# Optimization experiments

Hardware: AMD Instinct MI355X
Metric: run time of the kernel (lower is better)

The kernel has to match this reference:

```python
import jax, jax.numpy as jnp
import numpy as np

B, S, H, NH = 2, 384, 768, 12
DPH = H // NH
SCALE = 1.0 / np.sqrt(DPH)


def _layer_norm(x, g, b, eps=1e-6):
    m = jnp.mean(x, axis=-1, keepdims=True)
    v = jnp.mean(jnp.square(x - m), axis=-1, keepdims=True)
    return (x - m) * jax.lax.rsqrt(v + eps) * g + b


def setup_inputs() -> dict:
    key = jax.random.key(0)
    ks = jax.random.split(key, 12)
    std = 0.02
    return {
        "hidden_states": jax.random.normal(ks[0], (B, S, H), jnp.float32),
        "attention_mask": jnp.ones((B, S), jnp.int32),
        "rel_pos_embedding": jax.random.normal(ks[1], (B, S, S, H), jnp.float32),
        "Wq": jax.random.normal(ks[2], (H, H), jnp.float32) * std,
        "bq": jnp.zeros((H,), jnp.float32),
        "Wk": jax.random.normal(ks[3], (H, H), jnp.float32) * std,
        "bk": jnp.zeros((H,), jnp.float32),
        "Wv": jax.random.normal(ks[4], (H, H), jnp.float32) * std,
        "bv": jnp.zeros((H,), jnp.float32),
        "Wr": jax.random.normal(ks[5], (H, H), jnp.float32) * std,
        "br": jnp.zeros((H,), jnp.float32),
        "u": jax.random.normal(ks[6], (NH, DPH), jnp.float32) * std,
        "v": jax.random.normal(ks[7], (NH, DPH), jnp.float32) * std,
        "Wf": jax.random.normal(ks[8], (H, H), jnp.float32) * std,
        "bf": jnp.zeros((H,), jnp.float32),
        "ln_g": jnp.ones((H,), jnp.float32),
        "ln_b": jnp.zeros((H,), jnp.float32),
    }


def reference(hidden_states, attention_mask, rel_pos_embedding,
              Wq, bq, Wk, bk, Wv, bv, Wr, br, u, v, Wf, bf, ln_g, ln_b):
    # projections (torch Linear: x @ W.T + b)
    def heads(x):  # [B,S,H] -> [B,NH,S,DPH]
        return x.reshape(B, S, NH, DPH).transpose(0, 2, 1, 3)
    q = heads(hidden_states @ Wq.T + bq)
    k = heads(hidden_states @ Wk.T + bk)
    val = heads(hidden_states @ Wv.T + bv)
    # relative embedding projection: [B,S,S,H] -> [B,S,S,NH,DPH]
    rel = (rel_pos_embedding @ Wr.T + br).reshape(B, S, S, NH, DPH)

    # Transformer-XL style decomposition
    AC = jnp.einsum('bhid,bhjd->bhij', q + u[None, :, None, :], k)
    Bp = jnp.einsum('bhid,bijhd->bhij', q, rel)
    Dp = jnp.einsum('hd,bijhd->bhij', v, rel)
    scores = (AC + Bp + Dp) * SCALE

    # 2-D mask -> [B,1,1,S]
    ext = (1.0 - attention_mask[:, None, None, :].astype(scores.dtype)) * (-1e18)
    probs = jax.nn.softmax(scores + ext, axis=-1)  # dropout is identity at eval

    ctx = jnp.einsum('bhij,bhjd->bhid', probs, val)
    ctx = ctx.transpose(0, 2, 1, 3).reshape(B, S, H)
    out = ctx @ Wf.T + bf
    return _layer_norm(out + hidden_states, ln_g, ln_b)
```

## Files before the change

### kernel.cpp

```cpp
#include <hip/hip_runtime.h>
#include <cstddef>
#include <cstdint>

static constexpr int BB   = 2;
static constexpr int SS   = 384;
static constexpr int HH   = 768;
static constexpr int NHD  = 12;
static constexpr int ROWS = BB * SS;
#define SCALE_F 0.125f

typedef __attribute__((ext_vector_type(8))) short short8;
typedef __attribute__((ext_vector_type(4))) float f32x4;

static __device__ __forceinline__ unsigned short f2bf(float x) {
    unsigned int b = __float_as_uint(x);
    b = (b + 0x7fffu + ((b >> 16) & 1u)) >> 16;
    return (unsigned short)b;
}

__global__ __launch_bounds__(256) void k_tobf(const float* __restrict__ s0,
                                              const float* __restrict__ s1,
                                              const float* __restrict__ s2,
                                              const float* __restrict__ s3,
                                              const float* __restrict__ s4,
                                              unsigned short* __restrict__ d0,
                                              unsigned short* __restrict__ d1,
                                              unsigned short* __restrict__ d2,
                                              unsigned short* __restrict__ d3,
                                              unsigned short* __restrict__ d4) {
    const int z = blockIdx.y;
    const float* s = (z == 0) ? s0 : (z == 1) ? s1 : (z == 2) ? s2 : (z == 3) ? s3 : s4;
    unsigned short* d = (z == 0) ? d0 : (z == 1) ? d1 : (z == 2) ? d2 : (z == 3) ? d3 : d4;
    const int t = blockIdx.x * 256 + threadIdx.x;
    const float4 v = *(const float4*)&s[(size_t)t * 4];
    ushort4 o;
    o.x = f2bf(v.x); o.y = f2bf(v.y); o.z = f2bf(v.z); o.w = f2bf(v.w);
    *(ushort4*)&d[(size_t)t * 4] = o;
}

template<bool ADD>
__device__ __forceinline__ void mfma_gemm_body(const unsigned short* __restrict__ A,
                                               const unsigned short* __restrict__ W,
                                               const float* __restrict__ bias,
                                               const float* __restrict__ addsrc,
                                               float* __restrict__ C) {
    const int tid = threadIdx.x;
    const int wid = tid >> 6, lane = tid & 63;
    const int i0 = blockIdx.y * 64, o0 = blockIdx.x * 64;
    const int wr = (wid >> 1) * 32, wc = (wid & 1) * 32;
    const int lrow = lane & 15;
    const int kgrp = (lane >> 4) * 8;

    const unsigned short* Ar0 = A + (size_t)(i0 + wr + lrow) * HH + kgrp;
    const unsigned short* Ar1 = Ar0 + 16 * HH;
    const unsigned short* Wr0 = W + (size_t)(o0 + wc + lrow) * HH + kgrp;
    const unsigned short* Wr1 = Wr0 + 16 * HH;

    f32x4 acc00 = {0.f, 0.f, 0.f, 0.f}, acc01 = {0.f, 0.f, 0.f, 0.f};
    f32x4 acc10 = {0.f, 0.f, 0.f, 0.f}, acc11 = {0.f, 0.f, 0.f, 0.f};
#pragma unroll 4
    for (int k0 = 0; k0 < HH; k0 += 32) {
        const short8 a0 = *(const short8*)(Ar0 + k0);
        const short8 a1 = *(const short8*)(Ar1 + k0);
        const short8 b0 = *(const short8*)(Wr0 + k0);
        const short8 b1 = *(const short8*)(Wr1 + k0);
        acc00 = __builtin_amdgcn_mfma_f32_16x16x32_bf16(a0, b0, acc00, 0, 0, 0);
        acc01 = __builtin_amdgcn_mfma_f32_16x16x32_bf16(a0, b1, acc01, 0, 0, 0);
        acc10 = __builtin_amdgcn_mfma_f32_16x16x32_bf16(a1, b0, acc10, 0, 0, 0);
        acc11 = __builtin_amdgcn_mfma_f32_16x16x32_bf16(a1, b1, acc11, 0, 0, 0);
    }

    const int rbase = (lane >> 4) * 4;
#pragma unroll
    for (int tr = 0; tr < 2; tr++) {
#pragma unroll
        for (int tc = 0; tc < 2; tc++) {
            const f32x4 a = (tr == 0) ? ((tc == 0) ? acc00 : acc01)
                                      : ((tc == 0) ? acc10 : acc11);
            const int col = o0 + wc + tc * 16 + lrow;
            const float bv = bias[col];
#pragma unroll
            for (int r = 0; r < 4; r++) {
                const int row = i0 + wr + tr * 16 + rbase + r;
                float v = a[r] + bv;
                if (ADD) v += addsrc[(size_t)row * HH + col];
                C[(size_t)row * HH + col] = v;
            }
        }
    }
}

__global__ __launch_bounds__(256) void k_gemm_qkv(const unsigned short* __restrict__ A,
                                                  const unsigned short* __restrict__ Wq, const float* __restrict__ bq,
                                                  const unsigned short* __restrict__ Wk, const float* __restrict__ bk,
                                                  const unsigned short* __restrict__ Wv, const float* __restrict__ bv,
                                                  float* __restrict__ qo, float* __restrict__ ko,
                                                  float* __restrict__ vo) {
    const int z = blockIdx.z;
    const unsigned short* W = (z == 0) ? Wq : (z == 1) ? Wk : Wv;
    const float* bias = (z == 0) ? bq : (z == 1) ? bk : bv;
    float* C = (z == 0) ? qo : (z == 1) ? ko : vo;
    mfma_gemm_body<false>(A, W, bias, nullptr, C);
}

__global__ __launch_bounds__(256) void k_gemm_out(const unsigned short* __restrict__ A,
                                                  const unsigned short* __restrict__ W,
                                                  const float* __restrict__ bias,
                                                  const float* __restrict__ addsrc,
                                                  float* __restrict__ C) {
    mfma_gemm_body<true>(A, W, bias, addsrc, C);
}

__global__ __launch_bounds__(256) void k_uproj(const float* __restrict__ q,
                                               const float* __restrict__ Wr,
                                               const float* __restrict__ vhead,
                                               const float* __restrict__ br,
                                               unsigned short* __restrict__ U,
                                               float* __restrict__ cb) {
    const int h = blockIdx.z;
    const int e0 = blockIdx.x * 64, r0 = blockIdx.y * 64;
    __shared__ float qT[64][68];
    __shared__ float wE[64][68];
    const int tid = threadIdx.x;
    const int lr = tid >> 2;
    const int bc = (tid & 3) * 16;
#pragma unroll
    for (int m = 0; m < 4; m++) {
        const int col = bc + m * 4;
        const float4 qv = *(const float4*)&q[(size_t)(r0 + lr) * HH + h * 64 + col];
        const float4 vv = *(const float4*)&vhead[h * 64 + col];
        qT[col + 0][lr] = qv.x + vv.x;
        qT[col + 1][lr] = qv.y + vv.y;
        qT[col + 2][lr] = qv.z + vv.z;
        qT[col + 3][lr] = qv.w + vv.w;
        const float4 wv = *(const float4*)&Wr[(size_t)(h * 64 + lr) * HH + e0 + col];
        *(float4*)&wE[lr][col] = wv;
    }
    __syncthreads();
    const int tr = (tid >> 4) << 2;
    const int tc = (tid & 15) << 2;
    float acc[4][4] = {};
#pragma unroll 8
    for (int d = 0; d < 64; d++) {
        const float4 a4 = *(const float4*)&qT[d][tr];
        const float4 b4 = *(const float4*)&wE[d][tc];
        const float ab[4] = {a4.x, a4.y, a4.z, a4.w};
        const float bb[4] = {b4.x, b4.y, b4.z, b4.w};
#pragma unroll
        for (int r = 0; r < 4; r++)
#pragma unroll
            for (int c = 0; c < 4; c++)
                acc[r][c] = fmaf(ab[r], bb[c], acc[r][c]);
    }
#pragma unroll
    for (int r = 0; r < 4; r++) {
        ushort4 o;
        o.x = f2bf(acc[r][0]); o.y = f2bf(acc[r][1]);
        o.z = f2bf(acc[r][2]); o.w = f2bf(acc[r][3]);
        *(ushort4*)&U[(size_t)(r0 + tr + r) * (NHD * HH) + (size_t)h * HH + e0 + tc] = o;
    }
    if (e0 == 0 && tid < 64) {
        float s = 0.f;
        for (int d = 0; d < 64; d++)
            s = fmaf(qT[d][tid], br[h * 64 + d], s);
        cb[(r0 + tid) * NHD + h] = s;
    }
}

__global__ __launch_bounds__(256) void k_ac(const float* __restrict__ q,
                                            const float* __restrict__ kk,
                                            const float* __restrict__ uvec,
                                            const float* __restrict__ cb,
                                            float* __restrict__ sc) {
    const int bh = blockIdx.z;
    const int b = bh / NHD, h = bh - b * NHD;
    const int i0 = blockIdx.y * 64, j0 = blockIdx.x * 64;
    __shared__ float qT[64][68];
    __shared__ float kT[64][68];
    const int tid = threadIdx.x;
    const int lr = tid >> 2;
    const int bc = (tid & 3) * 16;
#pragma unroll
    for (int m = 0; m < 4; m++) {
        const int col = bc + m * 4;
        const float4 qv = *(const float4*)&q[(size_t)(b * SS + i0 + lr) * HH + h * 64 + col];
        const float4 uv = *(const float4*)&uvec[h * 64 + col];
        qT[col + 0][lr] = qv.x + uv.x;
        qT[col + 1][lr] = qv.y + uv.y;
        qT[col + 2][lr] = qv.z + uv.z;
        qT[col + 3][lr] = qv.w + uv.w;
        const float4 kv = *(const float4*)&kk[(size_t)(b * SS + j0 + lr) * HH + h * 64 + col];
        kT[col + 0][lr] = kv.x;
        kT[col + 1][lr] = kv.y;
        kT[col + 2][lr] = kv.z;
        kT[col + 3][lr] = kv.w;
    }
    __syncthreads();
    const int tr = (tid >> 4) << 2;
    const int tc = (tid & 15) << 2;
    float acc[4][4] = {};
#pragma unroll 8
    for (int d = 0; d < 64; d++) {
        const float4 a4 = *(const float4*)&qT[d][tr];
        const float4 b4 = *(const float4*)&kT[d][tc];
        const float ab[4] = {a4.x, a4.y, a4.z, a4.w};
        const float bb[4] = {b4.x, b4.y, b4.z, b4.w};
#pragma unroll
        for (int r = 0; r < 4; r++)
#pragma unroll
            for (int c = 0; c < 4; c++)
                acc[r][c] = fmaf(ab[r], bb[c], acc[r][c]);
    }
#pragma unroll
    for (int r = 0; r < 4; r++) {
        const int i = i0 + tr + r;
        const float cbr = cb[(b * SS + i) * NHD + h];
        float4 o;
        o.x = acc[r][0] + cbr; o.y = acc[r][1] + cbr;
        o.z = acc[r][2] + cbr; o.w = acc[r][3] + cbr;
        *(float4*)&sc[((size_t)(b * SS + i) * NHD + h) * SS + j0 + tc] = o;
    }
}

__global__ __launch_bounds__(256) void k_bd(const float* __restrict__ rpe,
                                            const unsigned short* __restrict__ U,
                                            const int* __restrict__ mask,
                                            float* __restrict__ scP) {
    const int i = blockIdx.x;
    const int b = blockIdx.y;
    const int row = b * SS + i;
    const int tid = threadIdx.x;

    __shared__ unsigned short Ul[NHD * HH];
    __shared__ float sc[NHD][392];
    __shared__ float extl[SS];

    float* plane = scP + (size_t)row * NHD * SS;

    {
        const uint4* Ur = (const uint4*)(U + (size_t)row * NHD * HH);
        uint4* Uld = (uint4*)Ul;
        for (int t = tid; t < NHD * HH / 8; t += 256) Uld[t] = Ur[t];
        for (int t = tid; t < NHD * 96; t += 256) {
            const int h = t / 96, c4 = (t - h * 96) << 2;
            *(float4*)&sc[h][c4] = *(const float4*)&plane[h * SS + c4];
        }
        for (int t = tid; t < SS; t += 256)
            extl[t] = (1.0f - (float)mask[b * SS + t]) * (-1e18f);
    }
    __syncthreads();

    const int wave = tid >> 6;
    const int lane = tid & 63;

    {
        const int jsub = lane >> 3;
        const int elane = lane & 7;
        const float* rrow = rpe + (size_t)row * SS * HH;

        for (int g = wave; g < 12; g += 4) {
            const int jbase = g * 32 + jsub;
            const float* rp0 = rrow + (size_t)jbase * HH + (elane << 2);
            float acc[4][NHD] = {};
#pragma unroll 2
            for (int ec = 0; ec < 24; ec++) {
                const int eo = ec << 5;
                const float4 t0 = *(const float4*)(rp0 + eo);
                const float4 t1 = *(const float4*)(rp0 + eo + 8 * HH);
                const float4 t2 = *(const float4*)(rp0 + eo + 16 * HH);
                const float4 t3 = *(const float4*)(rp0 + eo + 24 * HH);
                const float rb[4][4] = {{t0.x, t0.y, t0.z, t0.w},
                                        {t1.x, t1.y, t1.z, t1.w},
                                        {t2.x, t2.y, t2.z, t2.w},
                                        {t3.x, t3.y, t3.z, t3.w}};
                const int uo = eo + (elane << 2);
#pragma unroll
                for (int h = 0; h < NHD; h++) {
                    const uint2 w2 = *(const uint2*)&Ul[h * HH + uo];
                    float ub[4];
                    ub[0] = __uint_as_float(w2.x << 16);
                    ub[1] = __uint_as_float(w2.x & 0xffff0000u);
                    ub[2] = __uint_as_float(w2.y << 16);
                    ub[3] = __uint_as_float(w2.y & 0xffff0000u);
#pragma unroll
                    for (int rr = 0; rr < 4; rr++)
#pragma unroll
                        for (int c = 0; c < 4; c++)
                            acc[rr][h] = fmaf(rb[rr][c], ub[c], acc[rr][h]);
                }
            }
#pragma unroll
            for (int rr = 0; rr < 4; rr++)
#pragma unroll
                for (int h = 0; h < NHD; h++) {
                    float a = acc[rr][h];
                    a += __shfl_xor(a, 1);
                    a += __shfl_xor(a, 2);
                    a += __shfl_xor(a, 4);
                    acc[rr][h] = a;
                }
            if (elane == 0) {
#pragma unroll
                for (int rr = 0; rr < 4; rr++) {
                    const int j = jbase + (rr << 3);
#pragma unroll
                    for (int h = 0; h < NHD; h++)
                        sc[h][j] += acc[rr][h];
                }
            }
        }
    }
    __syncthreads();

    {
        for (int h = wave; h < NHD; h += 4) {
            float vbuf[6];
            float m = -1e30f;
#pragma unroll
            for (int t2 = 0; t2 < 6; t2++) {
                vbuf[t2] = sc[h][lane + t2 * 64] * SCALE_F + extl[lane + t2 * 64];
                m = fmaxf(m, vbuf[t2]);
            }
#pragma unroll
            for (int off = 1; off < 64; off <<= 1) m = fmaxf(m, __shfl_xor(m, off));
            float ssum = 0.f;
#pragma unroll
            for (int t2 = 0; t2 < 6; t2++) {
                const float e = __expf(vbuf[t2] - m);
                vbuf[t2] = e;
                ssum += e;
            }
#pragma unroll
            for (int off = 1; off < 64; off <<= 1) ssum += __shfl_xor(ssum, off);
            const float inv = 1.0f / ssum;
#pragma unroll
            for (int t2 = 0; t2 < 6; t2++)
                plane[h * SS + lane + t2 * 64] = vbuf[t2] * inv;
        }
    }
}

__global__ __launch_bounds__(256) void k_pv(const float* __restrict__ P,
                                            const float* __restrict__ val,
                                            unsigned short* __restrict__ ctxb) {
    const int bh = blockIdx.y;
    const int b = bh / NHD, h = bh - b * NHD;
    const int i0 = blockIdx.x * 64;
    __shared__ float pT[64][68];
    __shared__ float vB[64][68];
    const int tid = threadIdx.x;
    const int lr = tid >> 2;
    const int bc = (tid & 3) * 16;
    const int tr = (tid >> 4) << 2;
    const int tc = (tid & 15) << 2;

    float4 pv[4], vv[4];
#pragma unroll
    for (int m = 0; m < 4; m++) {
        const int col = bc + m * 4;
        pv[m] = *(const float4*)&P[((size_t)(b * SS + i0 + lr) * NHD + h) * SS + col];
        vv[m] = *(const float4*)&val[(size_t)(b * SS + lr) * HH + h * 64 + col];
    }
    float acc[4][4] = {};
    for (int jt = 0; jt < SS; jt += 64) {
        __syncthreads();
#pragma unroll
        for (int m = 0; m < 4; m++) {
            const int col = bc + m * 4;
            pT[col + 0][lr] = pv[m].x; pT[col + 1][lr] = pv[m].y;
            pT[col + 2][lr] = pv[m].z; pT[col + 3][lr] = pv[m].w;
            *(float4*)&vB[lr][col] = vv[m];
        }
        __syncthreads();
        if (jt + 64 < SS) {
#pragma unroll
            for (int m = 0; m < 4; m++) {
                const int col = bc + m * 4;
                pv[m] = *(const float4*)&P[((size_t)(b * SS + i0 + lr) * NHD + h) * SS + jt + 64 + col];
                vv[m] = *(const float4*)&val[(size_t)(b * SS + jt + 64 + lr) * HH + h * 64 + col];
            }
        }
#pragma unroll 8
        for (int jj = 0; jj < 64; jj++) {
            const float4 a4 = *(const float4*)&pT[jj][tr];
            const float4 b4 = *(const float4*)&vB[jj][tc];
            const float ab[4] = {a4.x, a4.y, a4.z, a4.w};
            const float bb[4] = {b4.x, b4.y, b4.z, b4.w};
#pragma unroll
            for (int r = 0; r < 4; r++)
#pragma unroll
                for (int c = 0; c < 4; c++)
                    acc[r][c] = fmaf(ab[r], bb[c], acc[r][c]);
        }
    }
#pragma unroll
    for (int r = 0; r < 4; r++) {
        ushort4 o;
        o.x = f2bf(acc[r][0]); o.y = f2bf(acc[r][1]);
        o.z = f2bf(acc[r][2]); o.w = f2bf(acc[r][3]);
        *(ushort4*)&ctxb[(size_t)(b * SS + i0 + tr + r) * HH + h * 64 + tc] = o;
    }
}

__global__ __launch_bounds__(256) void k_ln(const float* __restrict__ x,
                                            const float* __restrict__ g,
                                            const float* __restrict__ bta,
                                            float* __restrict__ o) {
    const int row = blockIdx.x;
    const int tid = threadIdx.x;
    const float* xr = x + (size_t)row * HH;
    __shared__ float red[4];
    const float v0 = xr[tid], v1 = xr[tid + 256], v2 = xr[tid + 512];
    float s = v0 + v1 + v2;
#pragma unroll
    for (int off = 1; off < 64; off <<= 1) s += __shfl_xor(s, off);
    if ((tid & 63) == 0) red[tid >> 6] = s;
    __syncthreads();
    const float mean = (red[0] + red[1] + red[2] + red[3]) * (1.0f / 768.0f);
    const float d0 = v0 - mean, d1 = v1 - mean, d2 = v2 - mean;
    float sq = d0 * d0 + d1 * d1 + d2 * d2;
#pragma unroll
    for (int off = 1; off < 64; off <<= 1) sq += __shfl_xor(sq, off);
    __syncthreads();
    if ((tid & 63) == 0) red[tid >> 6] = sq;
    __syncthreads();
    const float var = (red[0] + red[1] + red[2] + red[3]) * (1.0f / 768.0f);
    const float inv = rsqrtf(var + 1e-6f);
    o[(size_t)row * HH + tid]       = d0 * inv * g[tid]       + bta[tid];
    o[(size_t)row * HH + tid + 256] = d1 * inv * g[tid + 256] + bta[tid + 256];
    o[(size_t)row * HH + tid + 512] = d2 * inv * g[tid + 512] + bta[tid + 512];
}

extern "C" void kernel_launch(void* const* d_in, const int* in_sizes, int n_in,
                              void* d_out, int out_size, void* d_ws, size_t ws_size,
                              hipStream_t stream) {
    (void)in_sizes; (void)n_in; (void)out_size; (void)ws_size;
    const float* hs   = (const float*)d_in[0];
    const int*   mask = (const int*)d_in[1];
    const float* rpe  = (const float*)d_in[2];
    const float* Wq = (const float*)d_in[3];  const float* bq = (const float*)d_in[4];
    const float* Wk = (const float*)d_in[5];  const float* bk = (const float*)d_in[6];
    const float* Wv = (const float*)d_in[7];  const float* bv = (const float*)d_in[8];
    const float* Wr = (const float*)d_in[9];  const float* br = (const float*)d_in[10];
    const float* u  = (const float*)d_in[11]; const float* v  = (const float*)d_in[12];
    const float* Wf = (const float*)d_in[13]; const float* bf = (const float*)d_in[14];
    const float* lng = (const float*)d_in[15]; const float* lnb = (const float*)d_in[16];
    float* out = (float*)d_out;

    const size_t MAT = (size_t)ROWS * HH;
    float* wsf     = (float*)d_ws;
    float* q_ws    = wsf;
    float* k_ws    = q_ws   + MAT;
    float* v_ws    = k_ws   + MAT;
    float* lnin_ws = v_ws   + MAT;
    float* cb_ws   = lnin_ws + MAT;
    float* sc_ws   = cb_ws  + (size_t)ROWS * NHD;
    unsigned short* U_ws   = (unsigned short*)(sc_ws + (size_t)ROWS * NHD * SS);
    unsigned short* hs_b   = U_ws + (size_t)ROWS * NHD * HH;
    unsigned short* Wq_b   = hs_b + MAT;
    unsigned short* Wk_b   = Wq_b + MAT;
    unsigned short* Wv_b   = Wk_b + MAT;
    unsigned short* Wf_b   = Wv_b + MAT;
    unsigned short* ctx_b  = Wf_b + MAT;

    k_tobf<<<dim3(576, 5), 256, 0, stream>>>(hs, Wq, Wk, Wv, Wf,
                                             hs_b, Wq_b, Wk_b, Wv_b, Wf_b);
    k_gemm_qkv<<<dim3(12, 12, 3), 256, 0, stream>>>(hs_b, Wq_b, bq, Wk_b, bk, Wv_b, bv,
                                                    q_ws, k_ws, v_ws);
    k_uproj<<<dim3(12, 12, 12), 256, 0, stream>>>(q_ws, Wr, v, br, U_ws, cb_ws);
    k_ac<<<dim3(6, 6, 24), 256, 0, stream>>>(q_ws, k_ws, u, cb_ws, sc_ws);
    k_bd<<<dim3(SS, BB), 256, 0, stream>>>(rpe, U_ws, mask, sc_ws);
    k_pv<<<dim3(6, 24), 256, 0, stream>>>(sc_ws, v_ws, ctx_b);
    k_gemm_out<<<dim3(12, 12), 256, 0, stream>>>(ctx_b, Wf_b, bf, hs, lnin_ws);
    k_ln<<<dim3(768), 256, 0, stream>>>(lnin_ws, lng, lnb, out);
}
```

Baseline: 283.5 us.

## Port uproj, AC and PV stages to bf16 MFMA with bf16 intermediates

Replaces the fp32 FMA shared-memory tiles in the U-projection, AC score and P·V kernels with bf16 MFMA 16x16x32 tiles. The QKV GEMM now emits bf16 q+u, q+v, k and a transposed V directly, and Wr is transposed to bf16 in the conversion kernel. The cb bias term moves to a small separate kernel, and probabilities are written as bf16 for the PV stage. This cuts fp32 ALU work and intermediate memory traffic, at the cost of more bf16 rounding in the attention path.

```diff
diff --git a/kernel.cpp b/kernel.cpp
--- a/kernel.cpp
+++ b/kernel.cpp
@@ -17,33 +17,60 @@
     b = (b + 0x7fffu + ((b >> 16) & 1u)) >> 16;
     return (unsigned short)b;
 }
+static __device__ __forceinline__ float bf2f(unsigned short u) {
+    return __uint_as_float((unsigned int)u << 16);
+}
 
 __global__ __launch_bounds__(256) void k_tobf(const float* __restrict__ s0,
                                               const float* __restrict__ s1,
                                               const float* __restrict__ s2,
                                               const float* __restrict__ s3,
                                               const float* __restrict__ s4,
+                                              const float* __restrict__ Wr,
                                               unsigned short* __restrict__ d0,
                                               unsigned short* __restrict__ d1,
                                               unsigned short* __restrict__ d2,
                                               unsigned short* __restrict__ d3,
-                                              unsigned short* __restrict__ d4) {
+                                              unsigned short* __restrict__ d4,
+                                              unsigned short* __restrict__ WrT) {
+    __shared__ float t[32][33];
     const int z = blockIdx.y;
-    const float* s = (z == 0) ? s0 : (z == 1) ? s1 : (z == 2) ? s2 : (z == 3) ? s3 : s4;
-    unsigned short* d = (z == 0) ? d0 : (z == 1) ? d1 : (z == 2) ? d2 : (z == 3) ? d3 : d4;
-    const int t = blockIdx.x * 256 + threadIdx.x;
-    const float4 v = *(const float4*)&s[(size_t)t * 4];
-    ushort4 o;
-    o.x = f2bf(v.x); o.y = f2bf(v.y); o.z = f2bf(v.z); o.w = f2bf(v.w);
-    *(ushort4*)&d[(size_t)t * 4] = o;
-}
-
-template<bool ADD>
-__device__ __forceinline__ void mfma_gemm_body(const unsigned short* __restrict__ A,
-                                               const unsigned short* __restrict__ W,
-                                               const float* __restrict__ bias,
-                                               const float* __restrict__ addsrc,
-                                               float* __restrict__ C) {
+    if (z < 5) {
+        const float* s = (z == 0) ? s0 : (z == 1) ? s1 : (z == 2) ? s2 : (z == 3) ? s3 : s4;
+        unsigned short* d = (z == 0) ? d0 : (z == 1) ? d1 : (z == 2) ? d2 : (z == 3) ? d3 : d4;
+        const int tt = blockIdx.x * 256 + threadIdx.x;
+        const float4 v = *(const float4*)&s[(size_t)tt * 4];
+        ushort4 o;
+        o.x = f2bf(v.x); o.y = f2bf(v.y); o.z = f2bf(v.z); o.w = f2bf(v.w);
+        *(ushort4*)&d[(size_t)tt * 4] = o;
+    } else {
+        const int tile = blockIdx.x;
+        const int tr_ = tile / 24, tc_ = tile % 24;
+        const int r = threadIdx.x >> 3, c4 = (threadIdx.x & 7) * 4;
+        const float4 v = *(const float4*)&Wr[(size_t)(tr_ * 32 + r) * HH + tc_ * 32 + c4];
+        t[r][c4 + 0] = v.x; t[r][c4 + 1] = v.y; t[r][c4 + 2] = v.z; t[r][c4 + 3] = v.w;
+        __syncthreads();
+        ushort4 o;
+        o.x = f2bf(t[c4 + 0][r]); o.y = f2bf(t[c4 + 1][r]);
+        o.z = f2bf(t[c4 + 2][r]); o.w = f2bf(t[c4 + 3][r]);
+        *(ushort4*)&WrT[(size_t)(tc_ * 32 + r) * HH + tr_ * 32 + c4] = o;
+    }
+}
+
+__global__ __launch_bounds__(256) void k_gemm_qkv(const unsigned short* __restrict__ A,
+                                                  const unsigned short* __restrict__ Wqb, const float* __restrict__ bq,
+                                                  const unsigned short* __restrict__ Wkb, const float* __restrict__ bk,
+                                                  const unsigned short* __restrict__ Wvb, const float* __restrict__ bv,
+                                                  const float* __restrict__ uvec,
+                                                  const float* __restrict__ vvec,
+                                                  unsigned short* __restrict__ qu_b,
+                                                  unsigned short* __restrict__ qv_b,
+                                                  unsigned short* __restrict__ k_b,
+                                                  unsigned short* __restrict__ vT_b) {
+    const int z = blockIdx.z;
+    const unsigned short* W = (z == 0) ? Wqb : (z == 1) ? Wkb : Wvb;
+    const float* bias = (z == 0) ? bq : (z == 1) ? bk : bv;
+
     const int tid = threadIdx.x;
     const int wid = tid >> 6, lane = tid & 63;
     const int i0 = blockIdx.y * 64, o0 = blockIdx.x * 64;
@@ -56,8 +83,8 @@
     const unsigned short* Wr0 = W + (size_t)(o0 + wc + lrow) * HH + kgrp;
     const unsigned short* Wr1 = Wr0 + 16 * HH;
 
-    f32x4 acc00 = {0.f, 0.f, 0.f, 0.f}, acc01 = {0.f, 0.f, 0.f, 0.f};
-    f32x4 acc10 = {0.f, 0.f, 0.f, 0.f}, acc11 = {0.f, 0.f, 0.f, 0.f};
+    f32x4 acc00 = {0.f,0.f,0.f,0.f}, acc01 = {0.f,0.f,0.f,0.f};
+    f32x4 acc10 = {0.f,0.f,0.f,0.f}, acc11 = {0.f,0.f,0.f,0.f};
 #pragma unroll 4
     for (int k0 = 0; k0 < HH; k0 += 32) {
         const short8 a0 = *(const short8*)(Ar0 + k0);
@@ -78,154 +105,149 @@
             const f32x4 a = (tr == 0) ? ((tc == 0) ? acc00 : acc01)
                                       : ((tc == 0) ? acc10 : acc11);
             const int col = o0 + wc + tc * 16 + lrow;
-            const float bv = bias[col];
-#pragma unroll
-            for (int r = 0; r < 4; r++) {
-                const int row = i0 + wr + tr * 16 + rbase + r;
-                float v = a[r] + bv;
-                if (ADD) v += addsrc[(size_t)row * HH + col];
-                C[(size_t)row * HH + col] = v;
-            }
-        }
-    }
-}
-
-__global__ __launch_bounds__(256) void k_gemm_qkv(const unsigned short* __restrict__ A,
-                                                  const unsigned short* __restrict__ Wq, const float* __restrict__ bq,
-                                                  const unsigned short* __restrict__ Wk, const float* __restrict__ bk,
-                                                  const unsigned short* __restrict__ Wv, const float* __restrict__ bv,
-                                                  float* __restrict__ qo, float* __restrict__ ko,
-                                                  float* __restrict__ vo) {
-    const int z = blockIdx.z;
-    const unsigned short* W = (z == 0) ? Wq : (z == 1) ? Wk : Wv;
-    const float* bias = (z == 0) ? bq : (z == 1) ? bk : bv;
-    float* C = (z == 0) ? qo : (z == 1) ? ko : vo;
-    mfma_gemm_body<false>(A, W, bias, nullptr, C);
-}
-
-__global__ __launch_bounds__(256) void k_gemm_out(const unsigned short* __restrict__ A,
-                                                  const unsigned short* __restrict__ W,
-                                                  const float* __restrict__ bias,
-                                                  const float* __restrict__ addsrc,
-                                                  float* __restrict__ C) {
-    mfma_gemm_body<true>(A, W, bias, addsrc, C);
-}
-
-__global__ __launch_bounds__(256) void k_uproj(const float* __restrict__ q,
-                                               const float* __restrict__ Wr,
-                                               const float* __restrict__ vhead,
-                                               const float* __restrict__ br,
-                                               unsigned short* __restrict__ U,
-                                               float* __restrict__ cb) {
+            const float bvv = bias[col];
+            if (z == 0) {
+                const float uu = uvec[col], vv = vvec[col];
+#pragma unroll
+                for (int r = 0; r < 4; r++) {
+                    const int row = i0 + wr + tr * 16 + rbase + r;
+                    const float val = a[r] + bvv;
+                    qu_b[(size_t)row * HH + col] = f2bf(val + uu);
+                    qv_b[(size_t)row * HH + col] = f2bf(val + vv);
+                }
+            } else if (z == 1) {
+#pragma unroll
+                for (int r = 0; r < 4; r++) {
+                    const int row = i0 + wr + tr * 16 + rbase + r;
+                    k_b[(size_t)row * HH + col] = f2bf(a[r] + bvv);
+                }
+            } else {
+                const int row0 = i0 + wr + tr * 16 + rbase;
+                const int bb2 = row0 / SS;
+                const int jj0 = row0 - bb2 * SS;
+                const int h2 = col >> 6, d2 = col & 63;
+                ushort4 o;
+                o.x = f2bf(a[0] + bvv); o.y = f2bf(a[1] + bvv);
+                o.z = f2bf(a[2] + bvv); o.w = f2bf(a[3] + bvv);
+                *(ushort4*)&vT_b[((size_t)(bb2 * NHD + h2) * 64 + d2) * SS + jj0] = o;
+            }
+        }
+    }
+}
+
+__global__ void k_cb(const unsigned short* __restrict__ qv,
+                     const float* __restrict__ br, float* __restrict__ cb) {
+    const int t = blockIdx.x * 256 + threadIdx.x;
+    if (t >= ROWS * NHD) return;
+    const int row = t / NHD, h = t - row * NHD;
+    float s = 0.f;
+    for (int d = 0; d < 64; d++)
+        s = fmaf(bf2f(qv[(size_t)row * HH + h * 64 + d]), br[h * 64 + d], s);
+    cb[t] = s;
+}
+
+__global__ __launch_bounds__(256) void k_uproj(const unsigned short* __restrict__ qv,
+                                               const unsigned short* __restrict__ WrT,
+                                               unsigned short* __restrict__ U) {
     const int h = blockIdx.z;
     const int e0 = blockIdx.x * 64, r0 = blockIdx.y * 64;
-    __shared__ float qT[64][68];
-    __shared__ float wE[64][68];
-    const int tid = threadIdx.x;
-    const int lr = tid >> 2;
-    const int bc = (tid & 3) * 16;
-#pragma unroll
-    for (int m = 0; m < 4; m++) {
-        const int col = bc + m * 4;
-        const float4 qv = *(const float4*)&q[(size_t)(r0 + lr) * HH + h * 64 + col];
-        const float4 vv = *(const float4*)&vhead[h * 64 + col];
-        qT[col + 0][lr] = qv.x + vv.x;
-        qT[col + 1][lr] = qv.y + vv.y;
-        qT[col + 2][lr] = qv.z + vv.z;
-        qT[col + 3][lr] = qv.w + vv.w;
-        const float4 wv = *(const float4*)&Wr[(size_t)(h * 64 + lr) * HH + e0 + col];
-        *(float4*)&wE[lr][col] = wv;
-    }
-    __syncthreads();
-    const int tr = (tid >> 4) << 2;
-    const int tc = (tid & 15) << 2;
-    float acc[4][4] = {};
-#pragma unroll 8
-    for (int d = 0; d < 64; d++) {
-        const float4 a4 = *(const float4*)&qT[d][tr];
-        const float4 b4 = *(const float4*)&wE[d][tc];
-        const float ab[4] = {a4.x, a4.y, a4.z, a4.w};
-        const float bb[4] = {b4.x, b4.y, b4.z, b4.w};
-#pragma unroll
-        for (int r = 0; r < 4; r++)
-#pragma unroll
-            for (int c = 0; c < 4; c++)
-                acc[r][c] = fmaf(ab[r], bb[c], acc[r][c]);
-    }
-#pragma unroll
-    for (int r = 0; r < 4; r++) {
-        ushort4 o;
-        o.x = f2bf(acc[r][0]); o.y = f2bf(acc[r][1]);
-        o.z = f2bf(acc[r][2]); o.w = f2bf(acc[r][3]);
-        *(ushort4*)&U[(size_t)(r0 + tr + r) * (NHD * HH) + (size_t)h * HH + e0 + tc] = o;
-    }
-    if (e0 == 0 && tid < 64) {
-        float s = 0.f;
-        for (int d = 0; d < 64; d++)
-            s = fmaf(qT[d][tid], br[h * 64 + d], s);
-        cb[(r0 + tid) * NHD + h] = s;
-    }
-}
-
-__global__ __launch_bounds__(256) void k_ac(const float* __restrict__ q,
-                                            const float* __restrict__ kk,
-                                            const float* __restrict__ uvec,
+    const int tid = threadIdx.x;
+    const int wid = tid >> 6, lane = tid & 63;
+    const int wr = (wid >> 1) * 32, wc = (wid & 1) * 32;
+    const int lrow = lane & 15;
+    const int kgrp = (lane >> 4) * 8;
+
+    const unsigned short* Ar0 = qv + (size_t)(r0 + wr + lrow) * HH + h * 64 + kgrp;
+    const unsigned short* Ar1 = Ar0 + 16 * HH;
+    const unsigned short* Br0 = WrT + (size_t)(e0 + wc + lrow) * HH + h * 64 + kgrp;
+    const unsigned short* Br1 = Br0 + 16 * HH;
+
+    f32x4 acc00 = {0.f,0.f,0.f,0.f}, acc01 = {0.f,0.f,0.f,0.f};
+    f32x4 acc10 = {0.f,0.f,0.f,0.f}, acc11 = {0.f,0.f,0.f,0.f};
+#pragma unroll
+    for (int k0 = 0; k0 < 64; k0 += 32) {
+        const short8 a0 = *(const short8*)(Ar0 + k0);
+        const short8 a1 = *(const short8*)(Ar1 + k0);
+        const short8 b0 = *(const short8*)(Br0 + k0);
+        const short8 b1 = *(const short8*)(Br1 + k0);
+        acc00 = __builtin_amdgcn_mfma_f32_16x16x32_bf16(a0, b0, acc00, 0, 0, 0);
+        acc01 = __builtin_amdgcn_mfma_f32_16x16x32_bf16(a0, b1, acc01, 0, 0, 0);
+        acc10 = __builtin_amdgcn_mfma_f32_16x16x32_bf16(a1, b0, acc10, 0, 0, 0);
+        acc11 = __builtin_amdgcn_mfma_f32_16x16x32_bf16(a1, b1, acc11, 0, 0, 0);
+    }
+
+    const int rbase = (lane >> 4) * 4;
+#pragma unroll
+    for (int tr = 0; tr < 2; tr++) {
+#pragma unroll
+        for (int tc = 0; tc < 2; tc++) {
+            const f32x4 a = (tr == 0) ? ((tc == 0) ? acc00 : acc01)
+                                      : ((tc == 0) ? acc10 : acc11);
+            const int e = e0 + wc + tc * 16 + lrow;
+#pragma unroll
+            for (int r = 0; r < 4; r++) {
+                const int row = r0 + wr + tr * 16 + rbase + r;
+                U[(size_t)row * (NHD * HH) + (size_t)h * HH + e] = f2bf(a[r]);
+            }
+        }
+    }
+}
+
+__global__ __launch_bounds__(256) void k_ac(const unsigned short* __restrict__ qu,
+                                            const unsigned short* __restrict__ kb,
                                             const float* __restrict__ cb,
                                             float* __restrict__ sc) {
     const int bh = blockIdx.z;
     const int b = bh / NHD, h = bh - b * NHD;
     const int i0 = blockIdx.y * 64, j0 = blockIdx.x * 64;
-    __shared__ float qT[64][68];
-    __shared__ float kT[64][68];
-    const int tid = threadIdx.x;
-    const int lr = tid >> 2;
-    const int bc = (tid & 3) * 16;
-#pragma unroll
-    for (int m = 0; m < 4; m++) {
-        const int col = bc + m * 4;
-        const float4 qv = *(const float4*)&q[(size_t)(b * SS + i0 + lr) * HH + h * 64 + col];
-        const float4 uv = *(const float4*)&uvec[h * 64 + col];
-        qT[col + 0][lr] = qv.x + uv.x;
-        qT[col + 1][lr] = qv.y + uv.y;
-        qT[col + 2][lr] = qv.z + uv.z;
-        qT[col + 3][lr] = qv.w + uv.w;
-        const float4 kv = *(const float4*)&kk[(size_t)(b * SS + j0 + lr) * HH + h * 64 + col];
-        kT[col + 0][lr] = kv.x;
-        kT[col + 1][lr] = kv.y;
-        kT[col + 2][lr] = kv.z;
-        kT[col + 3][lr] = kv.w;
-    }
-    __syncthreads();
-    const int tr = (tid >> 4) << 2;
-    const int tc = (tid & 15) << 2;
-    float acc[4][4] = {};
-#pragma unroll 8
-    for (int d = 0; d < 64; d++) {
-        const float4 a4 = *(const float4*)&qT[d][tr];
-        const float4 b4 = *(const float4*)&kT[d][tc];
-        const float ab[4] = {a4.x, a4.y, a4.z, a4.w};
-        const float bb[4] = {b4.x, b4.y, b4.z, b4.w};
-#pragma unroll
-        for (int r = 0; r < 4; r++)
-#pragma unroll
-            for (int c = 0; c < 4; c++)
-                acc[r][c] = fmaf(ab[r], bb[c], acc[r][c]);
-    }
-#pragma unroll
-    for (int r = 0; r < 4; r++) {
-        const int i = i0 + tr + r;
-        const float cbr = cb[(b * SS + i) * NHD + h];
-        float4 o;
-        o.x = acc[r][0] + cbr; o.y = acc[r][1] + cbr;
-        o.z = acc[r][2] + cbr; o.w = acc[r][3] + cbr;
-        *(float4*)&sc[((size_t)(b * SS + i) * NHD + h) * SS + j0 + tc] = o;
+    const int tid = threadIdx.x;
+    const int wid = tid >> 6, lane = tid & 63;
+    const int wr = (wid >> 1) * 32, wc = (wid & 1) * 32;
+    const int lrow = lane & 15;
+    const int kgrp = (lane >> 4) * 8;
+
+    const unsigned short* Ar0 = qu + (size_t)(b * SS + i0 + wr + lrow) * HH + h * 64 + kgrp;
+    const unsigned short* Ar1 = Ar0 + 16 * HH;
+    const unsigned short* Br0 = kb + (size_t)(b * SS + j0 + wc + lrow) * HH + h * 64 + kgrp;
+    const unsigned short* Br1 = Br0 + 16 * HH;
+
+    f32x4 acc00 = {0.f,0.f,0.f,0.f}, acc01 = {0.f,0.f,0.f,0.f};
+    f32x4 acc10 = {0.f,0.f,0.f,0.f}, acc11 = {0.f,0.f,0.f,0.f};
+#pragma unroll
+    for (int k0 = 0; k0 < 64; k0 += 32) {
+        const short8 a0 = *(const short8*)(Ar0 + k0);
+        const short8 a1 = *(const short8*)(Ar1 + k0);
+        const short8 b0 = *(const short8*)(Br0 + k0);
+        const short8 b1 = *(const short8*)(Br1 + k0);
+        acc00 = __builtin_amdgcn_mfma_f32_16x16x32_bf16(a0, b0, acc00, 0, 0, 0);
+        acc01 = __builtin_amdgcn_mfma_f32_16x16x32_bf16(a0, b1, acc01, 0, 0, 0);
+        acc10 = __builtin_amdgcn_mfma_f32_16x16x32_bf16(a1, b0, acc10, 0, 0, 0);
+        acc11 = __builtin_amdgcn_mfma_f32_16x16x32_bf16(a1, b1, acc11, 0, 0, 0);
+    }
+
+    const int rbase = (lane >> 4) * 4;
+#pragma unroll
+    for (int tr = 0; tr < 2; tr++) {
+#pragma unroll
+        for (int tc = 0; tc < 2; tc++) {
+            const f32x4 a = (tr == 0) ? ((tc == 0) ? acc00 : acc01)
+                                      : ((tc == 0) ? acc10 : acc11);
+            const int j = j0 + wc + tc * 16 + lrow;
+#pragma unroll
+            for (int r = 0; r < 4; r++) {
+                const int i = i0 + wr + tr * 16 + rbase + r;
+                const float cbr = cb[(b * SS + i) * NHD + h];
+                sc[((size_t)(b * SS + i) * NHD + h) * SS + j] = a[r] + cbr;
+            }
+        }
     }
 }
 
 __global__ __launch_bounds__(256) void k_bd(const float* __restrict__ rpe,
                                             const unsigned short* __restrict__ U,
                                             const int* __restrict__ mask,
-                                            float* __restrict__ scP) {
+                                            const float* __restrict__ scin,
+                                            unsigned short* __restrict__ Pb) {
     const int i = blockIdx.x;
     const int b = blockIdx.y;
     const int row = b * SS + i;
@@ -235,7 +257,8 @@
     __shared__ float sc[NHD][392];
     __shared__ float extl[SS];
 
-    float* plane = scP + (size_t)row * NHD * SS;
+    const float* plane = scin + (size_t)row * NHD * SS;
+    unsigned short* pplane = Pb + (size_t)row * NHD * SS;
 
     {
         const uint4* Ur = (const uint4*)(U + (size_t)row * NHD * HH);
@@ -335,70 +358,105 @@
             const float inv = 1.0f / ssum;
 #pragma unroll
             for (int t2 = 0; t2 < 6; t2++)
-                plane[h * SS + lane + t2 * 64] = vbuf[t2] * inv;
-        }
-    }
-}
-
-__global__ __launch_bounds__(256) void k_pv(const float* __restrict__ P,
-                                            const float* __restrict__ val,
+                pplane[h * SS + lane + t2 * 64] = f2bf(vbuf[t2] * inv);
+        }
+    }
+}
+
+__global__ __launch_bounds__(256) void k_pv(const unsigned short* __restrict__ Pb,
+                                            const unsigned short* __restrict__ vTb,
                                             unsigned short* __restrict__ ctxb) {
     const int bh = blockIdx.y;
     const int b = bh / NHD, h = bh - b * NHD;
     const int i0 = blockIdx.x * 64;
-    __shared__ float pT[64][68];
-    __shared__ float vB[64][68];
-    const int tid = threadIdx.x;
-    const int lr = tid >> 2;
-    const int bc = (tid & 3) * 16;
-    const int tr = (tid >> 4) << 2;
-    const int tc = (tid & 15) << 2;
-
-    float4 pv[4], vv[4];
-#pragma unroll
-    for (int m = 0; m < 4; m++) {
-        const int col = bc + m * 4;
-        pv[m] = *(const float4*)&P[((size_t)(b * SS + i0 + lr) * NHD + h) * SS + col];
-        vv[m] = *(const float4*)&val[(size_t)(b * SS + lr) * HH + h * 64 + col];
-    }
-    float acc[4][4] = {};
-    for (int jt = 0; jt < SS; jt += 64) {
-        __syncthreads();
-#pragma unroll
-        for (int m = 0; m < 4; m++) {
-            const int col = bc + m * 4;
-            pT[col + 0][lr] = pv[m].x; pT[col + 1][lr] = pv[m].y;
-            pT[col + 2][lr] = pv[m].z; pT[col + 3][lr] = pv[m].w;
-            *(float4*)&vB[lr][col] = vv[m];
-        }
-        __syncthreads();
-        if (jt + 64 < SS) {
-#pragma unroll
-            for (int m = 0; m < 4; m++) {
-                const int col = bc + m * 4;
-                pv[m] = *(const float4*)&P[((size_t)(b * SS + i0 + lr) * NHD + h) * SS + jt + 64 + col];
-                vv[m] = *(const float4*)&val[(size_t)(b * SS + jt + 64 + lr) * HH + h * 64 + col];
-            }
-        }
-#pragma unroll 8
-        for (int jj = 0; jj < 64; jj++) {
-            const float4 a4 = *(const float4*)&pT[jj][tr];
-            const float4 b4 = *(const float4*)&vB[jj][tc];
-            const float ab[4] = {a4.x, a4.y, a4.z, a4.w};
-            const float bb[4] = {b4.x, b4.y, b4.z, b4.w};
-#pragma unroll
-            for (int r = 0; r < 4; r++)
-#pragma unroll
-                for (int c = 0; c < 4; c++)
-                    acc[r][c] = fmaf(ab[r], bb[c], acc[r][c]);
-        }
-    }
-#pragma unroll
-    for (int r = 0; r < 4; r++) {
-        ushort4 o;
-        o.x = f2bf(acc[r][0]); o.y = f2bf(acc[r][1]);
-        o.z = f2bf(acc[r][2]); o.w = f2bf(acc[r][3]);
-        *(ushort4*)&ctxb[(size_t)(b * SS + i0 + tr + r) * HH + h * 64 + tc] = o;
+    const int tid = threadIdx.x;
+    const int wid = tid >> 6, lane = tid & 63;
+    const int wr = (wid >> 1) * 32, wc = (wid & 1) * 32;
+    const int lrow = lane & 15;
+    const int kgrp = (lane >> 4) * 8;
+
+    const unsigned short* Ar0 = Pb + ((size_t)(b * SS + i0 + wr + lrow) * NHD + h) * SS + kgrp;
+    const unsigned short* Ar1 = Ar0 + (size_t)16 * NHD * SS;
+    const unsigned short* Br0 = vTb + ((size_t)(b * NHD + h) * 64 + wc + lrow) * SS + kgrp;
+    const unsigned short* Br1 = Br0 + 16 * SS;
+
+    f32x4 acc00 = {0.f,0.f,0.f,0.f}, acc01 = {0.f,0.f,0.f,0.f};
+    f32x4 acc10 = {0.f,0.f,0.f,0.f}, acc11 = {0.f,0.f,0.f,0.f};
+#pragma unroll 4
+    for (int k0 = 0; k0 < SS; k0 += 32) {
+        const short8 a0 = *(const short8*)(Ar0 + k0);
+        const short8 a1 = *(const short8*)(Ar1 + k0);
+        const short8 b0 = *(const short8*)(Br0 + k0);
+        const short8 b1 = *(const short8*)(Br1 + k0);
+        acc00 = __builtin_amdgcn_mfma_f32_16x16x32_bf16(a0, b0, acc00, 0, 0, 0);
+        acc01 = __builtin_amdgcn_mfma_f32_16x16x32_bf16(a0, b1, acc01, 0, 0, 0);
+        acc10 = __builtin_amdgcn_mfma_f32_16x16x32_bf16(a1, b0, acc10, 0, 0, 0);
+        acc11 = __builtin_amdgcn_mfma_f32_16x16x32_bf16(a1, b1, acc11, 0, 0, 0);
+    }
+
+    const int rbase = (lane >> 4) * 4;
+#pragma unroll
+    for (int tr = 0; tr < 2; tr++) {
+#pragma unroll
+        for (int tc = 0; tc < 2; tc++) {
+            const f32x4 a = (tr == 0) ? ((tc == 0) ? acc00 : acc01)
+                                      : ((tc == 0) ? acc10 : acc11);
+            const int d = wc + tc * 16 + lrow;
+#pragma unroll
+            for (int r = 0; r < 4; r++) {
+                const int row = b * SS + i0 + wr + tr * 16 + rbase + r;
+                ctxb[(size_t)row * HH + h * 64 + d] = f2bf(a[r]);
+            }
+        }
+    }
+}
+
+__global__ __launch_bounds__(256) void k_gemm_out(const unsigned short* __restrict__ A,
+                                                  const unsigned short* __restrict__ W,
+                                                  const float* __restrict__ bias,
+                                                  const float* __restrict__ addsrc,
+                                                  float* __restrict__ C) {
+    const int tid = threadIdx.x;
+    const int wid = tid >> 6, lane = tid & 63;
+    const int i0 = blockIdx.y * 64, o0 = blockIdx.x * 64;
+    const int wr = (wid >> 1) * 32, wc = (wid & 1) * 32;
+    const int lrow = lane & 15;
+    const int kgrp = (lane >> 4) * 8;
+
+    const unsigned short* Ar0 = A + (size_t)(i0 + wr + lrow) * HH + kgrp;
+    const unsigned short* Ar1 = Ar0 + 16 * HH;
+    const unsigned short* Wr0 = W + (size_t)(o0 + wc + lrow) * HH + kgrp;
+    const unsigned short* Wr1 = Wr0 + 16 * HH;
+
+    f32x4 acc00 = {0.f,0.f,0.f,0.f}, acc01 = {0.f,0.f,0.f,0.f};
+    f32x4 acc10 = {0.f,0.f,0.f,0.f}, acc11 = {0.f,0.f,0.f,0.f};
+#pragma unroll 4
+    for (int k0 = 0; k0 < HH; k0 += 32) {
+        const short8 a0 = *(const short8*)(Ar0 + k0);
+        const short8 a1 = *(const short8*)(Ar1 + k0);
+        const short8 b0 = *(const short8*)(Wr0 + k0);
+        const short8 b1 = *(const short8*)(Wr1 + k0);
+        acc00 = __builtin_amdgcn_mfma_f32_16x16x32_bf16(a0, b0, acc00, 0, 0, 0);
+        acc01 = __builtin_amdgcn_mfma_f32_16x16x32_bf16(a0, b1, acc01, 0, 0, 0);
+        acc10 = __builtin_amdgcn_mfma_f32_16x16x32_bf16(a1, b0, acc10, 0, 0, 0);
+        acc11 = __builtin_amdgcn_mfma_f32_16x16x32_bf16(a1, b1, acc11, 0, 0, 0);
+    }
+
+    const int rbase = (lane >> 4) * 4;
+#pragma unroll
+    for (int tr = 0; tr < 2; tr++) {
+#pragma unroll
+        for (int tc = 0; tc < 2; tc++) {
+            const f32x4 a = (tr == 0) ? ((tc == 0) ? acc00 : acc01)
+                                      : ((tc == 0) ? acc10 : acc11);
+            const int col = o0 + wc + tc * 16 + lrow;
+            const float bv = bias[col];
+#pragma unroll
+            for (int r = 0; r < 4; r++) {
+                const int row = i0 + wr + tr * 16 + rbase + r;
+                C[(size_t)row * HH + col] = a[r] + bv + addsrc[(size_t)row * HH + col];
+            }
+        }
     }
 }
 
@@ -449,28 +507,32 @@
 
     const size_t MAT = (size_t)ROWS * HH;
     float* wsf     = (float*)d_ws;
-    float* q_ws    = wsf;
-    float* k_ws    = q_ws   + MAT;
-    float* v_ws    = k_ws   + MAT;
-    float* lnin_ws = v_ws   + MAT;
-    float* cb_ws   = lnin_ws + MAT;
-    float* sc_ws   = cb_ws  + (size_t)ROWS * NHD;
-    unsigned short* U_ws   = (unsigned short*)(sc_ws + (size_t)ROWS * NHD * SS);
-    unsigned short* hs_b   = U_ws + (size_t)ROWS * NHD * HH;
-    unsigned short* Wq_b   = hs_b + MAT;
-    unsigned short* Wk_b   = Wq_b + MAT;
-    unsigned short* Wv_b   = Wk_b + MAT;
-    unsigned short* Wf_b   = Wv_b + MAT;
-    unsigned short* ctx_b  = Wf_b + MAT;
-
-    k_tobf<<<dim3(576, 5), 256, 0, stream>>>(hs, Wq, Wk, Wv, Wf,
-                                             hs_b, Wq_b, Wk_b, Wv_b, Wf_b);
+    float* lnin_ws = wsf;
+    float* sc_ws   = lnin_ws + MAT;
+    float* cb_ws   = sc_ws + (size_t)ROWS * NHD * SS;
+    unsigned short* U_ws  = (unsigned short*)(cb_ws + (size_t)ROWS * NHD);
+    unsigned short* hs_b  = U_ws + (size_t)ROWS * NHD * HH;
+    unsigned short* Wq_b  = hs_b + MAT;
+    unsigned short* Wk_b  = Wq_b + MAT;
+    unsigned short* Wv_b  = Wk_b + MAT;
+    unsigned short* Wf_b  = Wv_b + MAT;
+    unsigned short* WrT_b = Wf_b + MAT;
+    unsigned short* qu_b  = WrT_b + MAT;
+    unsigned short* qv_b  = qu_b + MAT;
+    unsigned short* k_b   = qv_b + MAT;
+    unsigned short* vT_b  = k_b + MAT;
+    unsigned short* ctx_b = vT_b + MAT;
+    unsigned short* P_b   = ctx_b + MAT;
+
+    k_tobf<<<dim3(576, 6), 256, 0, stream>>>(hs, Wq, Wk, Wv, Wf, Wr,
+                                             hs_b, Wq_b, Wk_b, Wv_b, Wf_b, WrT_b);
     k_gemm_qkv<<<dim3(12, 12, 3), 256, 0, stream>>>(hs_b, Wq_b, bq, Wk_b, bk, Wv_b, bv,
-                                                    q_ws, k_ws, v_ws);
-    k_uproj<<<dim3(12, 12, 12), 256, 0, stream>>>(q_ws, Wr, v, br, U_ws, cb_ws);
-    k_ac<<<dim3(6, 6, 24), 256, 0, stream>>>(q_ws, k_ws, u, cb_ws, sc_ws);
-    k_bd<<<dim3(SS, BB), 256, 0, stream>>>(rpe, U_ws, mask, sc_ws);
-    k_pv<<<dim3(6, 24), 256, 0, stream>>>(sc_ws, v_ws, ctx_b);
+                                                    u, v, qu_b, qv_b, k_b, vT_b);
+    k_cb<<<dim3(36), 256, 0, stream>>>(qv_b, br, cb_ws);
+    k_uproj<<<dim3(12, 12, 12), 256, 0, stream>>>(qv_b, WrT_b, U_ws);
+    k_ac<<<dim3(6, 6, 24), 256, 0, stream>>>(qu_b, k_b, cb_ws, sc_ws);
+    k_bd<<<dim3(SS, BB), 256, 0, stream>>>(rpe, U_ws, mask, sc_ws, P_b);
+    k_pv<<<dim3(6, 24), 256, 0, stream>>>(P_b, vT_b, ctx_b);
     k_gemm_out<<<dim3(12, 12), 256, 0, stream>>>(ctx_b, Wf_b, bf, hs, lnin_ws);
     k_ln<<<dim3(768), 256, 0, stream>>>(lnin_ws, lng, lnb, out);
 }
```

After: 262.8 us. 7.3% less time.
